# Kernel optimization log

Hardware: AMD Instinct MI355X
Metric: run time of the kernel (lower is better)

Reference implementation:

```python
import jax, jax.numpy as jnp
import numpy as np

# irreps: 16x0e + 8x1o ; sh: 1x0e + 1x1o
M0, M1 = 16, 8
N_NODES, N_EDGES, N_BASIS = 10000, 160000, 8
DIM = M0 + 3 * M1                      # 40
NW = M0*M0 + M0*M1 + M1*M1 + M1*M0     # 576 per-edge TP weights
LOG2 = 0.6931471805599453


def _split(x):
    return x[:, :M0], x[:, M0:].reshape(-1, M1, 3)


def _merge(xs, xv):
    return jnp.concatenate([xs, xv.reshape(xv.shape[0], -1)], axis=1)


def _lin(x, Ws, Wv):
    # e3nn o3.Linear: per-irrep channel mixing, 1/sqrt(fan_in) path norm
    xs, xv = _split(x)
    return _merge(xs @ Ws / np.sqrt(M0),
                  jnp.einsum('nui,uv->nvi', xv, Wv) / np.sqrt(M1))


def _ssp(x):  # ShiftedSoftPlus
    return jax.nn.softplus(x) - LOG2


def setup_inputs() -> dict:
    key = jax.random.key(0)
    k = jax.random.split(key, 14)
    return {
        'x': jax.random.normal(k[0], (N_NODES, DIM), jnp.float32),
        'edge_radial': jax.random.uniform(k[1], (N_EDGES, N_BASIS), dtype=jnp.float32),
        'edge_sh': jax.random.normal(k[2], (N_EDGES, 4), jnp.float32),
        'edge_src': jax.random.randint(k[3], (N_EDGES,), 0, N_NODES),
        'edge_dst': jax.random.randint(k[4], (N_EDGES,), 0, N_NODES),
        'n_nodes': N_NODES,
        'W1s': jax.random.normal(k[5], (M0, M0), jnp.float32),
        'W1v': jax.random.normal(k[6], (M1, M1), jnp.float32),
        'Wfc': jax.random.normal(k[7], (N_BASIS, NW), jnp.float32),
        'W2s': jax.random.normal(k[8], (M0, M0), jnp.float32),
        'W2v': jax.random.normal(k[9], (M1, M1), jnp.float32),
        'R00': jax.random.normal(k[10], (M0, M0, M0), jnp.float32),
        'R01': jax.random.normal(k[11], (M0, M1, M1), jnp.float32),
        'R10': jax.random.normal(k[12], (M1, M0, M1), jnp.float32),
        'R11': jax.random.normal(k[13], (M1, M1, M0), jnp.float32),
    }


def reference(x, edge_radial, edge_sh, edge_src, edge_dst, n_nodes,
              W1s, W1v, Wfc, W2s, W2v, R00, R01, R10, R11):
    inv2 = 1.0 / np.sqrt(2.0)

    # linear_1
    h = _lin(x, W1s, W1v)
    hs, hv = _split(h)

    # SO3Convolution: per-edge TP weights from radial net
    sh0, sh1 = edge_sh[:, 0], edge_sh[:, 1:4]
    w = edge_radial @ Wfc / np.sqrt(N_BASIS)  # [E, NW]
    o = 0
    w00 = w[:, o:o + M0*M0].reshape(-1, M0, M0); o += M0*M0  # 0e x 0e -> 0e
    w01 = w[:, o:o + M0*M1].reshape(-1, M0, M1); o += M0*M1  # 0e x 1o -> 1o
    w10 = w[:, o:o + M1*M1].reshape(-1, M1, M1); o += M1*M1  # 1o x 0e -> 1o
    w11 = w[:, o:o + M1*M0].reshape(-1, M1, M0)              # 1o x 1o -> 0e (CG: delta/sqrt(3))

    xs_e, xv_e = hs[edge_src], hv[edge_src]  # gather
    msg_s = (jnp.einsum('eu,e,euw->ew', xs_e, sh0, w00) / np.sqrt(M0)
             + jnp.einsum('eui,ei,euw->ew', xv_e, sh1, w11) / np.sqrt(3.0 * M1)) * inv2
    msg_v = (jnp.einsum('eu,ei,euw->ewi', xs_e, sh1, w01) / np.sqrt(M0)
             + jnp.einsum('eui,e,euw->ewi', xv_e, sh0, w10) / np.sqrt(M1)) * inv2

    deg = np.sqrt(N_EDGES / N_NODES)
    outs = jax.ops.segment_sum(msg_s, edge_dst, num_segments=n_nodes) / deg
    outv = jax.ops.segment_sum(msg_v, edge_dst, num_segments=n_nodes) / deg

    # linear_2
    h = _lin(_merge(outs, outv), W2s, W2v)
    hs, hv = _split(h)

    # NormActivation (normalize=True, ShiftedSoftPlus, eps=1e-8)
    eps = 1e-8
    ns = jnp.sqrt(hs * hs + eps * eps)
    hs = hs / ns * _ssp(ns)
    nv = jnp.sqrt(jnp.sum(hv * hv, -1, keepdims=True) + eps * eps)
    hv = hv / nv * _ssp(nv)
    out = _merge(hs, hv)

    # residual FullyConnectedTensorProduct(x, x)
    xs, xv = _split(x)
    rs = (jnp.einsum('nu,nv,uvw->nw', xs, xs, R00) / M0
          + jnp.einsum('nui,nvi,uvw->nw', xv, xv, R11) / np.sqrt(3.0 * M1 * M1)) * inv2
    rv = (jnp.einsum('nu,nvi,uvw->nwi', xs, xv, R01) / np.sqrt(M0 * M1)
          + jnp.einsum('nui,nv,uvw->nwi', xv, xs, R10) / np.sqrt(M1 * M0)) * inv2

    return out + _merge(rs, rv)
```

## Files before the change

### kernel.cpp

```cpp
#include <hip/hip_runtime.h>
#include <math.h>

constexpr int kM0 = 16, kM1 = 8, kDim = 40, kNW = 576;
constexpr int kNodes = 10000, kEdges = 160000;
constexpr int kCap = 96;
constexpr int kNB = 24;

__device__ __forceinline__ float sspf(float x){
  float ax = fabsf(x);
  return fmaxf(x, 0.f) + log1pf(expf(-ax)) - 0.69314718055994531f;
}

__global__ void __launch_bounds__(1024) k_setup(
    const float* __restrict__ Wfc, float* __restrict__ WfcT, int* __restrict__ cnt){
  int t = blockIdx.x*1024 + threadIdx.x;
  if (t < kNodes) cnt[t] = 0;
  if (t < kNW){
    #pragma unroll
    for (int b=0;b<8;++b) WfcT[t*8+b] = Wfc[b*kNW + t];
  }
}

__global__ void __launch_bounds__(512) k_edge(
    const float* __restrict__ er, const float* __restrict__ esh,
    const int* __restrict__ esrc, const int* __restrict__ edst,
    const float* __restrict__ x, const float* __restrict__ W1s,
    const float* __restrict__ W1v, const float* __restrict__ WfcT,
    float* __restrict__ msg, int* __restrict__ cnt){
  __shared__ float sh_x[64][41];
  __shared__ float sh_h[64][41];
  __shared__ int   smp[64];
  int t = threadIdx.x;
  int lane = t & 63;
  int q = __builtin_amdgcn_readfirstlane(t >> 6);
  int e0 = blockIdx.x*64;

  int myoff = 0;
  if (q == 0){
    int dst = edst[e0 + lane];
    int pos = atomicAdd(&cnt[dst], 1);
    myoff = (dst*kCap + pos)*kDim;
  }
  for (int idx = t; idx < 640; idx += 512){
    int el = idx/10, c4 = idx - el*10;
    int src = esrc[e0 + el];
    const float4 v = *(const float4*)(x + (size_t)src*kDim + c4*4);
    float* d = &sh_x[el][c4*4];
    d[0]=v.x; d[1]=v.y; d[2]=v.z; d[3]=v.w;
  }
  if (q == 0) smp[lane] = myoff;
  __syncthreads();

  {
    #pragma unroll
    for (int k=0;k<5;++k){
      const int c = q + 8*k;
      float o;
      if (c < 16){
        float acc=0.f;
        #pragma unroll
        for (int u=0;u<16;++u) acc += sh_x[lane][u]*W1s[u*16+c];
        o = acc*0.25f;
      } else {
        int j = c-16; int v = j/3, i = j-3*v;
        float acc=0.f;
        #pragma unroll
        for (int u=0;u<8;++u) acc += sh_x[lane][16+u*3+i]*W1v[u*8+v];
        o = acc*0.35355339059327373f;
      }
      sh_h[lane][c] = o;
    }
  }
  __syncthreads();

  int e = e0 + lane;
  float4 ra = *(const float4*)(er + (size_t)e*8);
  float4 rb = *(const float4*)(er + (size_t)e*8 + 4);
  const float r0=ra.x,r1=ra.y,r2=ra.z,r3=ra.w,r4=rb.x,r5=rb.y,r6=rb.z,r7=rb.w;
  float4 s4 = *(const float4*)(esh + (size_t)e*4);
  const float* hl = sh_h[lane];
  float* mp = msg + smp[lane];

#define DOT8(p) ((p)[0]*r0+(p)[1]*r1+(p)[2]*r2+(p)[3]*r3+(p)[4]*r4+(p)[5]*r5+(p)[6]*r6+(p)[7]*r7)

  const int w0 = q*2;
  float t00a=0.f, t00b=0.f, t11a=0.f, t11b=0.f;
  float t01=0.f, tx=0.f, ty=0.f, tz=0.f;

  #pragma unroll
  for (int u=0;u<16;++u){
    float xu = hl[u];
    const float* p0 = WfcT + (size_t)(u*16 + w0)*8;
    t00a += xu*DOT8(p0);
    t00b += xu*DOT8(p0 + 8);
    const float* p1 = WfcT + (size_t)(256 + u*8 + q)*8;
    t01 += xu*DOT8(p1);
  }
  #pragma unroll
  for (int u=0;u<8;++u){
    float v0=hl[16+u*3], v1=hl[16+u*3+1], v2=hl[16+u*3+2];
    float au = v0*s4.y + v1*s4.z + v2*s4.w;
    const float* p3 = WfcT + (size_t)(448 + u*16 + w0)*8;
    t11a += au*DOT8(p3);
    t11b += au*DOT8(p3 + 8);
    const float* p2 = WfcT + (size_t)(384 + u*8 + q)*8;
    float a = DOT8(p2);
    tx += v0*a; ty += v1*a; tz += v2*a;
  }
#undef DOT8

  constexpr float cs00 = 0.0625f;
  constexpr float cs11 = 0.05103103630798288f;
  constexpr float cv01 = 0.0625f;
  constexpr float cv10 = 0.08838834764831845f;

  *(float2*)(mp + w0) = make_float2(s4.x*t00a*cs00 + t11a*cs11,
                                    s4.x*t00b*cs00 + t11b*cs11);
  float va = t01*cv01, sc0 = s4.x*cv10;
  float* vp = mp + 16 + q*3;
  vp[0] = s4.y*va + tx*sc0;
  vp[1] = s4.z*va + ty*sc0;
  vp[2] = s4.w*va + tz*sc0;
}

__global__ void __launch_bounds__(960) k_node(
    const float* __restrict__ x, const float* __restrict__ msg,
    const int* __restrict__ cnt,
    const float* __restrict__ W2s, const float* __restrict__ W2v,
    const float* __restrict__ R00, const float* __restrict__ R01,
    const float* __restrict__ R10, const float* __restrict__ R11,
    float* __restrict__ out){
  __shared__ float sR00[4096], sR01[1024], sR10[1024], sR11[1024];
  __shared__ float sW2s[256], sW2v[64];
  __shared__ float sx[kNB][40], sa[kNB][40];
  __shared__ float4 sred[kNB][4][10];
  int t = threadIdx.x;
  for (int i=t; i<1024; i+=960) ((float4*)sR00)[i] = ((const float4*)R00)[i];
  if (t < 256){
    ((float4*)sR01)[t] = ((const float4*)R01)[t];
    ((float4*)sR10)[t] = ((const float4*)R10)[t];
    ((float4*)sR11)[t] = ((const float4*)R11)[t];
  }
  if (t >= 256 && t < 320) ((float4*)sW2s)[t-256] = ((const float4*)W2s)[t-256];
  if (t >= 320 && t < 336) ((float4*)sW2v)[t-320] = ((const float4*)W2v)[t-320];
  int nb = blockIdx.x*kNB;
  {
    int ns = t/40; int rem = t - ns*40; int kq = rem/10; int c4 = rem - kq*10;
    int n = nb + ns;
    float4 acc = make_float4(0.f,0.f,0.f,0.f);
    if (n < kNodes){
      int deg = cnt[n];
      const float* bp = msg + (size_t)n*kCap*kDim + c4*4;
      for (int k=kq; k<deg; k+=4){
        const float4 v = *(const float4*)(bp + (size_t)k*kDim);
        acc.x+=v.x; acc.y+=v.y; acc.z+=v.z; acc.w+=v.w;
      }
    }
    sred[ns][kq][c4] = acc;
  }
  __syncthreads();
  if (t < kNB*10){
    int ns = t/10, c4 = t - ns*10, n = nb+ns;
    float4 a0 = sred[ns][0][c4], a1 = sred[ns][1][c4];
    float4 a2 = sred[ns][2][c4], a3 = sred[ns][3][c4];
    sa[ns][c4*4+0] = (a0.x+a1.x+a2.x+a3.x)*0.25f;
    sa[ns][c4*4+1] = (a0.y+a1.y+a2.y+a3.y)*0.25f;
    sa[ns][c4*4+2] = (a0.z+a1.z+a2.z+a3.z)*0.25f;
    sa[ns][c4*4+3] = (a0.w+a1.w+a2.w+a3.w)*0.25f;
    float4 xv = (n < kNodes) ? *(const float4*)(x + (size_t)n*kDim + c4*4)
                             : make_float4(0.f,0.f,0.f,0.f);
    sx[ns][c4*4+0]=xv.x; sx[ns][c4*4+1]=xv.y; sx[ns][c4*4+2]=xv.z; sx[ns][c4*4+3]=xv.w;
  }
  __syncthreads();
  if (t < kNB*16){
    int ns = t>>4, w = t&15, n = nb+ns;
    const float* ap = sa[ns];
    const float* xp = sx[ns];
    float hsum = 0.f;
    #pragma unroll
    for (int u=0;u<16;++u) hsum += ap[u]*sW2s[u*16+w];
    hsum *= 0.25f;
    float nrm = sqrtf(hsum*hsum + 1e-16f);
    float val = hsum/nrm*sspf(nrm);
    float xs[16];
    #pragma unroll
    for (int v=0;v<16;++v) xs[v] = xp[v];
    float r0 = 0.f;
    #pragma unroll
    for (int u=0;u<16;++u){
      float tacc = 0.f;
      #pragma unroll
      for (int v=0;v<16;++v) tacc += xs[v]*sR00[(u*16+v)*16+w];
      r0 += xs[u]*tacc;
    }
    float xv[24];
    #pragma unroll
    for (int c2=0;c2<24;++c2) xv[c2] = xp[16+c2];
    float r1 = 0.f;
    #pragma unroll
    for (int u=0;u<8;++u){
      #pragma unroll
      for (int v=0;v<8;++v){
        float dot = xv[u*3]*xv[v*3] + xv[u*3+1]*xv[v*3+1] + xv[u*3+2]*xv[v*3+2];
        r1 += dot*sR11[(u*8+v)*16+w];
      }
    }
    if (n < kNodes)
      out[(size_t)n*kDim + w] = val + 0.04419417382415922f*r0 + 0.05103103630798288f*r1;
  } else if (t < kNB*16 + kNB*24) {
    int t2 = t - kNB*16;
    int ns = t2/24, cc = t2 - ns*24, w = cc/3, i = cc - w*3, n = nb+ns;
    const float* ap = sa[ns] + 16;
    const float* xp = sx[ns];
    float h0=0.f,h1=0.f,h2=0.f;
    #pragma unroll
    for (int u=0;u<8;++u){
      float wv = sW2v[u*8+w];
      h0 += ap[u*3+0]*wv; h1 += ap[u*3+1]*wv; h2 += ap[u*3+2]*wv;
    }
    const float sc = 0.35355339059327373f;
    h0*=sc; h1*=sc; h2*=sc;
    float nv = sqrtf(h0*h0+h1*h1+h2*h2 + 1e-16f);
    float hi = (i==0)?h0:((i==1)?h1:h2);
    float val = hi/nv*sspf(nv);
    float xs[16];
    #pragma unroll
    for (int v=0;v<16;++v) xs[v] = xp[v];
    float xvi[8];
    #pragma unroll
    for (int v=0;v<8;++v) xvi[v] = xp[16+v*3+i];
    float racc = 0.f;
    #pragma unroll
    for (int u=0;u<16;++u){
      float tacc=0.f;
      #pragma unroll
      for (int v=0;v<8;++v) tacc += xvi[v]*sR01[(u*8+v)*8+w];
      racc += xs[u]*tacc;
    }
    #pragma unroll
    for (int u=0;u<8;++u){
      float tacc=0.f;
      #pragma unroll
      for (int v=0;v<16;++v) tacc += xs[v]*sR10[(u*16+v)*8+w];
      racc += xvi[u]*tacc;
    }
    if (n < kNodes)
      out[(size_t)n*kDim + 16 + cc] = val + 0.0625f*racc;
  }
}

extern "C" void kernel_launch(void* const* d_in, const int* in_sizes, int n_in,
                              void* d_out, int out_size, void* d_ws, size_t ws_size,
                              hipStream_t stream){
  const float* x   = (const float*)d_in[0];
  const float* er  = (const float*)d_in[1];
  const float* esh = (const float*)d_in[2];
  const int*   esrc= (const int*)d_in[3];
  const int*   edst= (const int*)d_in[4];
  const float* W1s = (const float*)d_in[6];
  const float* W1v = (const float*)d_in[7];
  const float* Wfc = (const float*)d_in[8];
  const float* W2s = (const float*)d_in[9];
  const float* W2v = (const float*)d_in[10];
  const float* R00 = (const float*)d_in[11];
  const float* R01 = (const float*)d_in[12];
  const float* R10 = (const float*)d_in[13];
  const float* R11 = (const float*)d_in[14];
  float* out = (float*)d_out;

  char* wsb = (char*)d_ws;
  float* msg  = (float*)wsb;
  float* WfcT = msg + (size_t)kNodes*kCap*kDim;
  int*   cnt  = (int*)(WfcT + (size_t)kNW*8);

  k_setup<<<10, 1024, 0, stream>>>(Wfc, WfcT, cnt);
  k_edge<<<kEdges/64, 512, 0, stream>>>(er, esh, esrc, edst, x, W1s, W1v, WfcT, msg, cnt);
  k_node<<<(kNodes+kNB-1)/kNB, 960, 0, stream>>>(x, msg, cnt, W2s, W2v, R00, R01, R10, R11, out);
}
```

Measured before the change: 149.7 us.

## Shrink node blocks to 8 nodes and gather messages per scalar column

Result: no change. 152.7 us (+2.0%).

```diff
diff --git a/kernel.cpp b/kernel.cpp
--- a/kernel.cpp
+++ b/kernel.cpp
@@ -4,7 +4,7 @@
 constexpr int kM0 = 16, kM1 = 8, kDim = 40, kNW = 576;
 constexpr int kNodes = 10000, kEdges = 160000;
 constexpr int kCap = 96;
-constexpr int kNB = 24;
+constexpr int kNB = 8;
 
 __device__ __forceinline__ float sspf(float x){
   float ax = fabsf(x);
@@ -123,7 +123,7 @@
   vp[2] = s4.w*va + tz*sc0;
 }
 
-__global__ void __launch_bounds__(960) k_node(
+__global__ void __launch_bounds__(320) k_node(
     const float* __restrict__ x, const float* __restrict__ msg,
     const int* __restrict__ cnt,
     const float* __restrict__ W2s, const float* __restrict__ W2v,
@@ -133,43 +133,33 @@
   __shared__ float sR00[4096], sR01[1024], sR10[1024], sR11[1024];
   __shared__ float sW2s[256], sW2v[64];
   __shared__ float sx[kNB][40], sa[kNB][40];
-  __shared__ float4 sred[kNB][4][10];
   int t = threadIdx.x;
-  for (int i=t; i<1024; i+=960) ((float4*)sR00)[i] = ((const float4*)R00)[i];
+  #pragma unroll
+  for (int i=0;i<4;++i) ((float4*)sR00)[t + i*320] = ((const float4*)R00)[t + i*320];
   if (t < 256){
     ((float4*)sR01)[t] = ((const float4*)R01)[t];
     ((float4*)sR10)[t] = ((const float4*)R10)[t];
     ((float4*)sR11)[t] = ((const float4*)R11)[t];
-  }
-  if (t >= 256 && t < 320) ((float4*)sW2s)[t-256] = ((const float4*)W2s)[t-256];
-  if (t >= 320 && t < 336) ((float4*)sW2v)[t-320] = ((const float4*)W2v)[t-320];
+  } else {
+    ((float4*)sW2s)[t-256] = ((const float4*)W2s)[t-256];
+  }
+  if (t < 16) ((float4*)sW2v)[t] = ((const float4*)W2v)[t];
   int nb = blockIdx.x*kNB;
   {
-    int ns = t/40; int rem = t - ns*40; int kq = rem/10; int c4 = rem - kq*10;
-    int n = nb + ns;
-    float4 acc = make_float4(0.f,0.f,0.f,0.f);
-    if (n < kNodes){
-      int deg = cnt[n];
-      const float* bp = msg + (size_t)n*kCap*kDim + c4*4;
-      for (int k=kq; k<deg; k+=4){
-        const float4 v = *(const float4*)(bp + (size_t)k*kDim);
-        acc.x+=v.x; acc.y+=v.y; acc.z+=v.z; acc.w+=v.w;
-      }
-    }
-    sred[ns][kq][c4] = acc;
-  }
-  __syncthreads();
-  if (t < kNB*10){
-    int ns = t/10, c4 = t - ns*10, n = nb+ns;
-    float4 a0 = sred[ns][0][c4], a1 = sred[ns][1][c4];
-    float4 a2 = sred[ns][2][c4], a3 = sred[ns][3][c4];
-    sa[ns][c4*4+0] = (a0.x+a1.x+a2.x+a3.x)*0.25f;
-    sa[ns][c4*4+1] = (a0.y+a1.y+a2.y+a3.y)*0.25f;
-    sa[ns][c4*4+2] = (a0.z+a1.z+a2.z+a3.z)*0.25f;
-    sa[ns][c4*4+3] = (a0.w+a1.w+a2.w+a3.w)*0.25f;
-    float4 xv = (n < kNodes) ? *(const float4*)(x + (size_t)n*kDim + c4*4)
-                             : make_float4(0.f,0.f,0.f,0.f);
-    sx[ns][c4*4+0]=xv.x; sx[ns][c4*4+1]=xv.y; sx[ns][c4*4+2]=xv.z; sx[ns][c4*4+3]=xv.w;
+    int ns = t/40, c = t - ns*40, n = nb + ns;
+    int deg = cnt[n];
+    const float* bp = msg + (size_t)n*kCap*kDim + c;
+    float a0=0.f,a1=0.f,a2=0.f,a3=0.f;
+    int k=0;
+    for (; k+4<=deg; k+=4){
+      a0 += bp[(size_t)(k+0)*kDim];
+      a1 += bp[(size_t)(k+1)*kDim];
+      a2 += bp[(size_t)(k+2)*kDim];
+      a3 += bp[(size_t)(k+3)*kDim];
+    }
+    for (; k<deg; ++k) a0 += bp[(size_t)k*kDim];
+    sa[ns][c] = ((a0+a1)+(a2+a3))*0.25f;
+    sx[ns][c] = x[(size_t)n*kDim + c];
   }
   __syncthreads();
   if (t < kNB*16){
@@ -205,9 +195,8 @@
         r1 += dot*sR11[(u*8+v)*16+w];
       }
     }
-    if (n < kNodes)
-      out[(size_t)n*kDim + w] = val + 0.04419417382415922f*r0 + 0.05103103630798288f*r1;
-  } else if (t < kNB*16 + kNB*24) {
+    out[(size_t)n*kDim + w] = val + 0.04419417382415922f*r0 + 0.05103103630798288f*r1;
+  } else {
     int t2 = t - kNB*16;
     int ns = t2/24, cc = t2 - ns*24, w = cc/3, i = cc - w*3, n = nb+ns;
     const float* ap = sa[ns] + 16;
@@ -244,8 +233,7 @@
       for (int v=0;v<16;++v) tacc += xs[v]*sR10[(u*16+v)*8+w];
       racc += xvi[u]*tacc;
     }
-    if (n < kNodes)
-      out[(size_t)n*kDim + 16 + cc] = val + 0.0625f*racc;
+    out[(size_t)n*kDim + 16 + cc] = val + 0.0625f*racc;
   }
 }
 
@@ -275,5 +263,5 @@
 
   k_setup<<<10, 1024, 0, stream>>>(Wfc, WfcT, cnt);
   k_edge<<<kEdges/64, 512, 0, stream>>>(er, esh, esrc, edst, x, W1s, W1v, WfcT, msg, cnt);
-  k_node<<<(kNodes+kNB-1)/kNB, 960, 0, stream>>>(x, msg, cnt, W2s, W2v, R00, R01, R10, R11, out);
-}
+  k_node<<<kNodes/kNB, 320, 0, stream>>>(x, msg, cnt, W2s, W2v, R00, R01, R10, R11, out);
+}
```

## Compute per-edge tensor-product contractions with bf16 MFMA instead of scalar FMA

Applied to the files above, without the earlier changes.

New measurement: 133.9 us. -10.5%, faster.

```diff
diff --git a/kernel.cpp b/kernel.cpp
--- a/kernel.cpp
+++ b/kernel.cpp
@@ -1,4 +1,5 @@
 #include <hip/hip_runtime.h>
+#include <hip/hip_bf16.h>
 #include <math.h>
 
 constexpr int kM0 = 16, kM1 = 8, kDim = 40, kNW = 576;
@@ -6,121 +7,173 @@
 constexpr int kCap = 96;
 constexpr int kNB = 24;
 
+typedef __attribute__((ext_vector_type(8))) short short8;
+typedef __attribute__((ext_vector_type(4))) float f32x4;
+
 __device__ __forceinline__ float sspf(float x){
   float ax = fabsf(x);
   return fmaxf(x, 0.f) + log1pf(expf(-ax)) - 0.69314718055994531f;
 }
 
+__device__ __forceinline__ short bfbits(float f){
+  unsigned u = __float_as_uint(f);
+  u += 0x7fffu + ((u >> 16) & 1u);
+  return (short)(u >> 16);
+}
+
 __global__ void __launch_bounds__(1024) k_setup(
-    const float* __restrict__ Wfc, float* __restrict__ WfcT, int* __restrict__ cnt){
+    const float* __restrict__ Wfc, short* __restrict__ Bf, int* __restrict__ cnt){
   int t = blockIdx.x*1024 + threadIdx.x;
   if (t < kNodes) cnt[t] = 0;
-  if (t < kNW){
-    #pragma unroll
-    for (int b=0;b<8;++b) WfcT[t*8+b] = Wfc[b*kNW + t];
-  }
-}
-
-__global__ void __launch_bounds__(512) k_edge(
+  if (t < 12*64*8){
+    int s = t >> 9, l = (t >> 3) & 63, j = t & 7;
+    int n = l & 15, kg = l >> 4;
+    float val = 0.f;
+    if (s < 4){
+      int k = s*32 + kg*8 + j, u = k>>3, b = k&7;
+      val = Wfc[b*kNW + u*16 + n];
+    } else if (s < 8){
+      int k = (s-4)*32 + kg*8 + j, u = k>>3, b = k&7;
+      if (n < 8) val = Wfc[b*kNW + 256 + u*8 + n];
+    } else if (s < 10){
+      int k = (s-8)*32 + kg*8 + j, u = k>>3, b = k&7;
+      val = Wfc[b*kNW + 448 + u*16 + n];
+    } else {
+      int k = (s-10)*32 + kg*8 + j, u = k>>3, b = k&7;
+      if (n < 8) val = Wfc[b*kNW + 384 + u*8 + n];
+    }
+    Bf[t] = bfbits(val);
+  }
+}
+
+__global__ void __launch_bounds__(256, 4) k_edge(
     const float* __restrict__ er, const float* __restrict__ esh,
     const int* __restrict__ esrc, const int* __restrict__ edst,
     const float* __restrict__ x, const float* __restrict__ W1s,
-    const float* __restrict__ W1v, const float* __restrict__ WfcT,
+    const float* __restrict__ W1v, const short* __restrict__ Bf,
     float* __restrict__ msg, int* __restrict__ cnt){
   __shared__ float sh_x[64][41];
   __shared__ float sh_h[64][41];
+  __shared__ float sh_r[64][12];
+  __shared__ float sh_s[64][4];
+  __shared__ float sh_au[64][9];
   __shared__ int   smp[64];
-  int t = threadIdx.x;
-  int lane = t & 63;
-  int q = __builtin_amdgcn_readfirstlane(t >> 6);
+  int t = threadIdx.x, lane = t & 63;
+  int wv = __builtin_amdgcn_readfirstlane(t >> 6);
   int e0 = blockIdx.x*64;
 
-  int myoff = 0;
-  if (q == 0){
+  if (wv == 0){
     int dst = edst[e0 + lane];
     int pos = atomicAdd(&cnt[dst], 1);
-    myoff = (dst*kCap + pos)*kDim;
-  }
-  for (int idx = t; idx < 640; idx += 512){
+    smp[lane] = (dst*kCap + pos)*kDim;
+  }
+  for (int idx = t; idx < 640; idx += 256){
     int el = idx/10, c4 = idx - el*10;
-    int src = esrc[e0 + el];
-    const float4 v = *(const float4*)(x + (size_t)src*kDim + c4*4);
+    float4 v = *(const float4*)(x + (size_t)esrc[e0+el]*kDim + c4*4);
     float* d = &sh_x[el][c4*4];
     d[0]=v.x; d[1]=v.y; d[2]=v.z; d[3]=v.w;
   }
-  if (q == 0) smp[lane] = myoff;
-  __syncthreads();
-
-  {
-    #pragma unroll
-    for (int k=0;k<5;++k){
-      const int c = q + 8*k;
-      float o;
-      if (c < 16){
-        float acc=0.f;
-        #pragma unroll
-        for (int u=0;u<16;++u) acc += sh_x[lane][u]*W1s[u*16+c];
-        o = acc*0.25f;
-      } else {
-        int j = c-16; int v = j/3, i = j-3*v;
-        float acc=0.f;
-        #pragma unroll
-        for (int u=0;u<8;++u) acc += sh_x[lane][16+u*3+i]*W1v[u*8+v];
-        o = acc*0.35355339059327373f;
-      }
-      sh_h[lane][c] = o;
-    }
-  }
-  __syncthreads();
-
-  int e = e0 + lane;
-  float4 ra = *(const float4*)(er + (size_t)e*8);
-  float4 rb = *(const float4*)(er + (size_t)e*8 + 4);
-  const float r0=ra.x,r1=ra.y,r2=ra.z,r3=ra.w,r4=rb.x,r5=rb.y,r6=rb.z,r7=rb.w;
-  float4 s4 = *(const float4*)(esh + (size_t)e*4);
-  const float* hl = sh_h[lane];
-  float* mp = msg + smp[lane];
-
-#define DOT8(p) ((p)[0]*r0+(p)[1]*r1+(p)[2]*r2+(p)[3]*r3+(p)[4]*r4+(p)[5]*r5+(p)[6]*r6+(p)[7]*r7)
-
-  const int w0 = q*2;
-  float t00a=0.f, t00b=0.f, t11a=0.f, t11b=0.f;
-  float t01=0.f, tx=0.f, ty=0.f, tz=0.f;
-
-  #pragma unroll
-  for (int u=0;u<16;++u){
-    float xu = hl[u];
-    const float* p0 = WfcT + (size_t)(u*16 + w0)*8;
-    t00a += xu*DOT8(p0);
-    t00b += xu*DOT8(p0 + 8);
-    const float* p1 = WfcT + (size_t)(256 + u*8 + q)*8;
-    t01 += xu*DOT8(p1);
-  }
-  #pragma unroll
-  for (int u=0;u<8;++u){
-    float v0=hl[16+u*3], v1=hl[16+u*3+1], v2=hl[16+u*3+2];
-    float au = v0*s4.y + v1*s4.z + v2*s4.w;
-    const float* p3 = WfcT + (size_t)(448 + u*16 + w0)*8;
-    t11a += au*DOT8(p3);
-    t11b += au*DOT8(p3 + 8);
-    const float* p2 = WfcT + (size_t)(384 + u*8 + q)*8;
-    float a = DOT8(p2);
-    tx += v0*a; ty += v1*a; tz += v2*a;
-  }
-#undef DOT8
+  if (t < 128){
+    int e = t>>1, hf = t&1;
+    float4 v = *(const float4*)(er + (size_t)(e0+e)*8 + hf*4);
+    *(float4*)&sh_r[e][hf*4] = v;
+  } else if (t < 192){
+    int e = t-128;
+    float4 v = *(const float4*)(esh + (size_t)(e0+e)*4);
+    *(float4*)&sh_s[e][0] = v;
+  }
+  __syncthreads();
+  #pragma unroll
+  for (int k=0;k<10;++k){
+    const int c = wv + 4*k;
+    float o;
+    if (c < 16){
+      float acc=0.f;
+      #pragma unroll
+      for (int u=0;u<16;++u) acc += sh_x[lane][u]*W1s[u*16+c];
+      o = acc*0.25f;
+    } else {
+      int j = c-16; int v = j/3, i = j-3*v;
+      float acc=0.f;
+      #pragma unroll
+      for (int u=0;u<8;++u) acc += sh_x[lane][16+u*3+i]*W1v[u*8+v];
+      o = acc*0.35355339059327373f;
+    }
+    sh_h[lane][c] = o;
+  }
+  __syncthreads();
+  for (int idx = t; idx < 512; idx += 256){
+    int e = idx>>3, u = idx&7;
+    sh_au[e][u] = sh_h[e][16+u*3+0]*sh_s[e][1]
+                + sh_h[e][16+u*3+1]*sh_s[e][2]
+                + sh_h[e][16+u*3+2]*sh_s[e][3];
+  }
+  __syncthreads();
+
+  const int n = lane & 15, kg = lane >> 4;
+  const int erow = wv*16 + n;
+  float4 ra = *(const float4*)&sh_r[erow][0];
+  float4 rb = *(const float4*)&sh_r[erow][4];
+  float rr[8] = {ra.x,ra.y,ra.z,ra.w,rb.x,rb.y,rb.z,rb.w};
+  const short8* Bp = (const short8*)Bf;
+  short8 b00[4], b01[4], b11[2], b10[2];
+  #pragma unroll
+  for (int m=0;m<4;++m){ b00[m] = Bp[m*64+lane]; b01[m] = Bp[(4+m)*64+lane]; }
+  #pragma unroll
+  for (int m=0;m<2;++m){ b11[m] = Bp[(8+m)*64+lane]; b10[m] = Bp[(10+m)*64+lane]; }
+
+  f32x4 d00 = {0.f,0.f,0.f,0.f}, d01 = {0.f,0.f,0.f,0.f}, d11 = {0.f,0.f,0.f,0.f};
+  f32x4 d10_0 = {0.f,0.f,0.f,0.f}, d10_1 = {0.f,0.f,0.f,0.f}, d10_2 = {0.f,0.f,0.f,0.f};
+
+  #pragma unroll
+  for (int m=0;m<4;++m){
+    float hsv = sh_h[erow][4*m + kg];
+    short8 a;
+    #pragma unroll
+    for (int j=0;j<8;++j) a[j] = bfbits(hsv*rr[j]);
+    d00 = __builtin_amdgcn_mfma_f32_16x16x32_bf16(a, b00[m], d00, 0, 0, 0);
+    d01 = __builtin_amdgcn_mfma_f32_16x16x32_bf16(a, b01[m], d01, 0, 0, 0);
+  }
+  #pragma unroll
+  for (int m=0;m<2;++m){
+    float auv = sh_au[erow][4*m + kg];
+    short8 a;
+    #pragma unroll
+    for (int j=0;j<8;++j) a[j] = bfbits(auv*rr[j]);
+    d11 = __builtin_amdgcn_mfma_f32_16x16x32_bf16(a, b11[m], d11, 0, 0, 0);
+  }
+  #pragma unroll
+  for (int m=0;m<2;++m){
+    float h0v = sh_h[erow][16 + (4*m+kg)*3 + 0];
+    float h1v = sh_h[erow][16 + (4*m+kg)*3 + 1];
+    float h2v = sh_h[erow][16 + (4*m+kg)*3 + 2];
+    short8 a0, a1, a2;
+    #pragma unroll
+    for (int j=0;j<8;++j){
+      a0[j] = bfbits(h0v*rr[j]); a1[j] = bfbits(h1v*rr[j]); a2[j] = bfbits(h2v*rr[j]);
+    }
+    d10_0 = __builtin_amdgcn_mfma_f32_16x16x32_bf16(a0, b10[m], d10_0, 0, 0, 0);
+    d10_1 = __builtin_amdgcn_mfma_f32_16x16x32_bf16(a1, b10[m], d10_1, 0, 0, 0);
+    d10_2 = __builtin_amdgcn_mfma_f32_16x16x32_bf16(a2, b10[m], d10_2, 0, 0, 0);
+  }
 
   constexpr float cs00 = 0.0625f;
   constexpr float cs11 = 0.05103103630798288f;
   constexpr float cv01 = 0.0625f;
   constexpr float cv10 = 0.08838834764831845f;
-
-  *(float2*)(mp + w0) = make_float2(s4.x*t00a*cs00 + t11a*cs11,
-                                    s4.x*t00b*cs00 + t11b*cs11);
-  float va = t01*cv01, sc0 = s4.x*cv10;
-  float* vp = mp + 16 + q*3;
-  vp[0] = s4.y*va + tx*sc0;
-  vp[1] = s4.z*va + ty*sc0;
-  vp[2] = s4.w*va + tz*sc0;
+  #pragma unroll
+  for (int reg=0;reg<4;++reg){
+    int el = wv*16 + kg*4 + reg;
+    float* mp = msg + smp[el];
+    float s0 = sh_s[el][0];
+    mp[n] = s0*cs00*d00[reg] + cs11*d11[reg];
+    if (n < 8){
+      float dv = cv01*d01[reg], sv = s0*cv10;
+      mp[16+3*n+0] = sh_s[el][1]*dv + sv*d10_0[reg];
+      mp[16+3*n+1] = sh_s[el][2]*dv + sv*d10_1[reg];
+      mp[16+3*n+2] = sh_s[el][3]*dv + sv*d10_2[reg];
+    }
+  }
 }
 
 __global__ void __launch_bounds__(960) k_node(
@@ -269,11 +322,11 @@
   float* out = (float*)d_out;
 
   char* wsb = (char*)d_ws;
-  float* msg  = (float*)wsb;
-  float* WfcT = msg + (size_t)kNodes*kCap*kDim;
-  int*   cnt  = (int*)(WfcT + (size_t)kNW*8);
-
-  k_setup<<<10, 1024, 0, stream>>>(Wfc, WfcT, cnt);
-  k_edge<<<kEdges/64, 512, 0, stream>>>(er, esh, esrc, edst, x, W1s, W1v, WfcT, msg, cnt);
+  float* msg = (float*)wsb;
+  short* Bf  = (short*)(wsb + (size_t)kNodes*kCap*kDim*4);
+  int*   cnt = (int*)(Bf + 12*64*8);
+
+  k_setup<<<10, 1024, 0, stream>>>(Wfc, Bf, cnt);
+  k_edge<<<kEdges/64, 256, 0, stream>>>(er, esh, esrc, edst, x, W1s, W1v, Bf, msg, cnt);
   k_node<<<(kNodes+kNB-1)/kNB, 960, 0, stream>>>(x, msg, cnt, W2s, W2v, R00, R01, R10, R11, out);
 }
```
